# Optimization experiments

Measured on AMD Instinct MI355X. Metric: run time of the kernel, lower is better.

The kernel has to match this reference:

```python
import jax, jax.numpy as jnp
import numpy as np

B, C, D = 2048, 1000, 256


def setup_inputs() -> dict:
    key = jax.random.key(0)
    k1, k2 = jax.random.split(key)
    x = jax.random.normal(k1, (B, D), dtype=jnp.float32)
    # xavier_uniform for prototypes [C, D]: bound = sqrt(6 / (C + D))
    bound = np.sqrt(6.0 / (C + D)).astype(np.float32)
    prototypes = jax.random.uniform(k2, (C, D), dtype=jnp.float32,
                                    minval=-bound, maxval=bound)
    log_diag = jnp.zeros((C, D), dtype=jnp.float32)
    return {"x": x, "prototypes": prototypes, "log_diag": log_diag}


def reference(x, prototypes, log_diag):
    # diff: [B, C, D] broadcast of x against class prototypes
    diff = x[:, None, :] - prototypes[None, :, :]
    precision_diag = jnp.exp(log_diag)  # [C, D]
    # per-class diagonal-weighted squared distance, reduced over features
    mahalanobis_sq = jnp.sum(diff * diff * precision_diag[None, :, :], axis=2)  # [B, C]
    return -mahalanobis_sq
```

## Files before the change

### kernel.cpp

```cpp
#include <hip/hip_runtime.h>
#include <hip/hip_bf16.h>


#define C_N 1000
#define D_N 256

typedef __attribute__((ext_vector_type(8))) short bf16x8;
typedef __attribute__((ext_vector_type(4))) float f32x4;

__device__ inline bf16x8 pack8(const float* v) {
  union { bf16x8 o; __hip_bfloat162 h[4]; } u;
#pragma unroll
  for (int j = 0; j < 4; ++j)
    u.h[j] = __float22bfloat162_rn(make_float2(v[2 * j], v[2 * j + 1]));
  return u.o;
}

__global__ __launch_bounds__(512, 2) void mahal_fused(
    const float* __restrict__ x, const float* __restrict__ p,
    const float* __restrict__ ld, float* __restrict__ out) {
  __shared__ short lB[4][16][64][8];
  __shared__ float s_lds[2][64];

  const int tid = threadIdx.x;
  const int w   = tid >> 6;
  const int l   = tid & 63;
  const int r16 = l & 15;
  const int hi  = l >> 4;
  const int bx  = blockIdx.x;
  const int by  = blockIdx.y;

  {
    const int ct = w & 3;
    const int dh = w >> 2;
    const int c  = by * 64 + ct * 16 + r16;
    const bool valid = (c < C_N);
    float sp = 0.f;
#pragma unroll
    for (int t = 0; t < 4; ++t) {
      const int d = dh * 128 + t * 32 + hi * 8;
      float wv[8], pwv[8];
      if (valid) {
        const float* lp = ld + (size_t)c * D_N + d;
        const float* pp = p  + (size_t)c * D_N + d;
        float4 l0 = *reinterpret_cast<const float4*>(lp);
        float4 l1 = *reinterpret_cast<const float4*>(lp + 4);
        float4 p0 = *reinterpret_cast<const float4*>(pp);
        float4 p1 = *reinterpret_cast<const float4*>(pp + 4);
        float lv[8] = {l0.x,l0.y,l0.z,l0.w,l1.x,l1.y,l1.z,l1.w};
        float pv[8] = {p0.x,p0.y,p0.z,p0.w,p1.x,p1.y,p1.z,p1.w};
#pragma unroll
        for (int j = 0; j < 8; ++j) {
          float wj = __expf(lv[j]);
          wv[j]  = wj;
          pwv[j] = -2.f * pv[j] * wj;
          sp += pv[j] * pv[j] * wj;
        }
      } else {
#pragma unroll
        for (int j = 0; j < 8; ++j) { wv[j] = 0.f; pwv[j] = 0.f; }
      }
      *reinterpret_cast<bf16x8*>(&lB[ct][dh * 4 + t][l][0])     = pack8(wv);
      *reinterpret_cast<bf16x8*>(&lB[ct][8 + dh * 4 + t][l][0]) = pack8(pwv);
    }
    sp += __shfl_xor(sp, 16, 64);
    sp += __shfl_xor(sp, 32, 64);
    if (l < 16) s_lds[dh][ct * 16 + r16] = sp;
  }

  bf16x8 aSq[8], aRaw[8];
  {
    const int row = bx * 128 + w * 16 + r16;
#pragma unroll
    for (int t = 0; t < 8; ++t) {
      const int d = t * 32 + hi * 8;
      const float* xp = x + (size_t)row * D_N + d;
      float4 v0 = *reinterpret_cast<const float4*>(xp);
      float4 v1 = *reinterpret_cast<const float4*>(xp + 4);
      float v[8] = {v0.x,v0.y,v0.z,v0.w,v1.x,v1.y,v1.z,v1.w};
      float sq[8];
#pragma unroll
      for (int j = 0; j < 8; ++j) sq[j] = v[j] * v[j];
      aSq[t]  = pack8(sq);
      aRaw[t] = pack8(v);
    }
  }
  __syncthreads();

  f32x4 acc0[4], acc1[4];
#pragma unroll
  for (int n = 0; n < 4; ++n) { acc0[n] = {0.f,0.f,0.f,0.f}; acc1[n] = {0.f,0.f,0.f,0.f}; }

#pragma unroll
  for (int kt = 0; kt < 8; ++kt) {
#pragma unroll
    for (int n = 0; n < 4; ++n) {
      bf16x8 b0 = *reinterpret_cast<const bf16x8*>(&lB[n][kt][l][0]);
      bf16x8 b1 = *reinterpret_cast<const bf16x8*>(&lB[n][8 + kt][l][0]);
      acc0[n] = __builtin_amdgcn_mfma_f32_16x16x32_bf16(aSq[kt],  b0, acc0[n], 0, 0, 0);
      acc1[n] = __builtin_amdgcn_mfma_f32_16x16x32_bf16(aRaw[kt], b1, acc1[n], 0, 0, 0);
    }
  }

  const int rowbase = bx * 128 + w * 16 + hi * 4;
#pragma unroll
  for (int n = 0; n < 4; ++n) {
    const int col = by * 64 + n * 16 + r16;
    if (col < C_N) {
      const int ci = n * 16 + r16;
      const float sc = s_lds[0][ci] + s_lds[1][ci];
#pragma unroll
      for (int r = 0; r < 4; ++r)
        out[(size_t)(rowbase + r) * C_N + col] = -(acc0[n][r] + acc1[n][r] + sc);
    }
  }
}

extern "C" void kernel_launch(void* const* d_in, const int* in_sizes, int n_in,
                              void* d_out, int out_size, void* d_ws, size_t ws_size,
                              hipStream_t stream) {
  const float* x  = (const float*)d_in[0];
  const float* p  = (const float*)d_in[1];
  const float* ld = (const float*)d_in[2];
  float* out = (float*)d_out;
  mahal_fused<<<dim3(16, 16), 512, 0, stream>>>(x, p, ld, out);
}
```

Baseline: 16.09 us.

## Retile waves to 2x2 MFMA subtiles to halve LDS B-operand reads

Each wave now computes a 32-row by 32-column subtile (two M tiles by two N tiles) instead of 16 rows by all 64 columns. Every B fragment read from LDS is reused across two A row tiles, which halves per-wave LDS traffic for the B operand. In exchange each wave loads and converts twice as many x rows from global memory, so x traffic per block doubles and A-fragment register use goes up.

```diff
diff --git a/kernel.cpp b/kernel.cpp
--- a/kernel.cpp
+++ b/kernel.cpp
@@ -68,9 +68,12 @@
     if (l < 16) s_lds[dh][ct * 16 + r16] = sp;
   }
 
-  bf16x8 aSq[8], aRaw[8];
-  {
-    const int row = bx * 128 + w * 16 + r16;
+  const int wm = w >> 1;
+  const int wn = w & 1;
+  bf16x8 aSq[2][8], aRaw[2][8];
+#pragma unroll
+  for (int mt = 0; mt < 2; ++mt) {
+    const int row = bx * 128 + wm * 32 + mt * 16 + r16;
 #pragma unroll
     for (int t = 0; t < 8; ++t) {
       const int d = t * 32 + hi * 8;
@@ -81,37 +84,45 @@
       float sq[8];
 #pragma unroll
       for (int j = 0; j < 8; ++j) sq[j] = v[j] * v[j];
-      aSq[t]  = pack8(sq);
-      aRaw[t] = pack8(v);
+      aSq[mt][t]  = pack8(sq);
+      aRaw[mt][t] = pack8(v);
     }
   }
   __syncthreads();
 
-  f32x4 acc0[4], acc1[4];
+  f32x4 accS[2][2], accR[2][2];
 #pragma unroll
-  for (int n = 0; n < 4; ++n) { acc0[n] = {0.f,0.f,0.f,0.f}; acc1[n] = {0.f,0.f,0.f,0.f}; }
+  for (int mt = 0; mt < 2; ++mt)
+#pragma unroll
+    for (int n = 0; n < 2; ++n) { accS[mt][n] = {0.f,0.f,0.f,0.f}; accR[mt][n] = {0.f,0.f,0.f,0.f}; }
 
 #pragma unroll
   for (int kt = 0; kt < 8; ++kt) {
 #pragma unroll
-    for (int n = 0; n < 4; ++n) {
-      bf16x8 b0 = *reinterpret_cast<const bf16x8*>(&lB[n][kt][l][0]);
-      bf16x8 b1 = *reinterpret_cast<const bf16x8*>(&lB[n][8 + kt][l][0]);
-      acc0[n] = __builtin_amdgcn_mfma_f32_16x16x32_bf16(aSq[kt],  b0, acc0[n], 0, 0, 0);
-      acc1[n] = __builtin_amdgcn_mfma_f32_16x16x32_bf16(aRaw[kt], b1, acc1[n], 0, 0, 0);
+    for (int n = 0; n < 2; ++n) {
+      bf16x8 b0 = *reinterpret_cast<const bf16x8*>(&lB[wn * 2 + n][kt][l][0]);
+      bf16x8 b1 = *reinterpret_cast<const bf16x8*>(&lB[wn * 2 + n][8 + kt][l][0]);
+#pragma unroll
+      for (int mt = 0; mt < 2; ++mt) {
+        accS[mt][n] = __builtin_amdgcn_mfma_f32_16x16x32_bf16(aSq[mt][kt],  b0, accS[mt][n], 0, 0, 0);
+        accR[mt][n] = __builtin_amdgcn_mfma_f32_16x16x32_bf16(aRaw[mt][kt], b1, accR[mt][n], 0, 0, 0);
+      }
     }
   }
 
-  const int rowbase = bx * 128 + w * 16 + hi * 4;
 #pragma unroll
-  for (int n = 0; n < 4; ++n) {
-    const int col = by * 64 + n * 16 + r16;
-    if (col < C_N) {
-      const int ci = n * 16 + r16;
-      const float sc = s_lds[0][ci] + s_lds[1][ci];
+  for (int mt = 0; mt < 2; ++mt) {
+    const int rowbase = bx * 128 + wm * 32 + mt * 16 + hi * 4;
 #pragma unroll
-      for (int r = 0; r < 4; ++r)
-        out[(size_t)(rowbase + r) * C_N + col] = -(acc0[n][r] + acc1[n][r] + sc);
+    for (int n = 0; n < 2; ++n) {
+      const int col = by * 64 + wn * 32 + n * 16 + r16;
+      if (col < C_N) {
+        const int ci = wn * 32 + n * 16 + r16;
+        const float sc = s_lds[0][ci] + s_lds[1][ci];
+#pragma unroll
+        for (int r = 0; r < 4; ++r)
+          out[(size_t)(rowbase + r) * C_N + col] = -(accS[mt][n][r] + accR[mt][n][r] + sc);
+      }
     }
   }
 }
```

Result: slower. 19.50 us (+21.2%).
